# Kernel optimization log

Measured on AMD Instinct MI355X. Metric: run time of the kernel, lower is better.

## Reference

```python
import jax, jax.numpy as jnp
import numpy as np

N = 50000      # nodes
DIM = 128      # feature dim
H = 4          # heads
C = DIM // H   # per-head channels
E = 800000     # edges (before self-loops)
LRELU_SLOPE = 0.2
LN_EPS = 1e-5


def setup_inputs() -> dict:
    key = jax.random.key(0)
    ks = jax.random.split(key, 12)
    def p(k, shape, scale=0.05):
        return jax.random.normal(k, shape, jnp.float32) * scale
    return {
        "x": jax.random.normal(ks[0], (N, DIM), jnp.float32),
        "edge_index": jax.random.randint(ks[1], (2, E), 0, N),
        "W1": p(ks[2], (DIM, DIM)), "b1": jnp.zeros((DIM,), jnp.float32),
        "att_src1": p(ks[3], (H, C)), "att_dst1": p(ks[4], (H, C)),
        "W2": p(ks[5], (DIM, DIM)), "b2": jnp.zeros((DIM,), jnp.float32),
        "att_src2": p(ks[6], (H, C)), "att_dst2": p(ks[7], (H, C)),
        "gate_W": p(ks[8], (2 * DIM, 2)), "gate_b": jnp.zeros((2,), jnp.float32),
        "ln_gamma": jnp.ones((DIM,), jnp.float32), "ln_beta": jnp.zeros((DIM,), jnp.float32),
    }


def _gat(x, src, dst, W, b, a_src, a_dst):
    # Linear transform, split heads: [N, H, C]
    h = (x @ W).reshape(-1, H, C)
    # Per-node attention logits per head: [N, H]
    e_src = jnp.einsum("nhc,hc->nh", h, a_src)
    e_dst = jnp.einsum("nhc,hc->nh", h, a_dst)
    # Per-edge logits (edge j->i: src=j, dst=i): [E, H]
    e = jax.nn.leaky_relu(e_src[src] + e_dst[dst], LRELU_SLOPE)
    # Segment softmax over edges sharing a destination (self-loops guarantee >=1 edge/node)
    m = jax.ops.segment_max(e, dst, num_segments=N)
    p = jnp.exp(e - m[dst])
    s = jax.ops.segment_sum(p, dst, num_segments=N)
    alpha = p / s[dst]                                   # [E, H]
    # Weighted scatter-add aggregation
    out = jax.ops.segment_sum(h[src] * alpha[..., None], dst, num_segments=N)
    return out.reshape(-1, H * C) + b                    # [N, DIM]


def reference(x, edge_index, W1, b1, att_src1, att_dst1, W2, b2, att_src2, att_dst2,
              gate_W, gate_b, ln_gamma, ln_beta):
    n = x.shape[0]
    loops = jnp.arange(n, dtype=edge_index.dtype)
    src = jnp.concatenate([edge_index[0], loops])  # PyG GATConv add_self_loops=True
    dst = jnp.concatenate([edge_index[1], loops])
    out1 = _gat(x, src, dst, W1, b1, att_src1, att_dst1)
    out2 = _gat(x, src, dst, W2, b2, att_src2, att_dst2)
    gate = jax.nn.softmax(jnp.concatenate([out1, out2], axis=-1) @ gate_W + gate_b, axis=-1)
    out = gate[:, 0:1] * out1 + gate[:, 1:2] * out2
    # residual + LayerNorm (dropout is identity in eval)
    y = x + out
    mu = jnp.mean(y, axis=-1, keepdims=True)
    var = jnp.var(y, axis=-1, keepdims=True)
    return (y - mu) * jax.lax.rsqrt(var + LN_EPS) * ln_gamma + ln_beta
```

## Files before the change

### kernel.cpp

```cpp
#include <hip/hip_runtime.h>
#include <hip/hip_bf16.h>


typedef unsigned short u16;
typedef __bf16 bf16x8 __attribute__((ext_vector_type(8)));
typedef float f32x4 __attribute__((ext_vector_type(4)));

#define LRELU_SLOPE 0.2f
#define LN_EPS 1e-5f
#define SH 8

__device__ __forceinline__ float bfbits(unsigned int hi_bits) {
    union { unsigned int i; float f; } v; v.i = hi_bits; return v.f;
}
__device__ __forceinline__ float bflo(unsigned int u) { return bfbits(u << 16); }
__device__ __forceinline__ float bfhi(unsigned int u) { return bfbits(u & 0xFFFF0000u); }
__device__ __forceinline__ u16 f2bf(float f) {
    union { float f; unsigned int i; } v; v.f = f;
    unsigned int lsb = (v.i >> 16) & 1u;
    v.i += 0x7FFFu + lsb;
    return (u16)(v.i >> 16);
}

__global__ void k_prep(const float* __restrict__ W1, const float* __restrict__ W2,
                       u16* __restrict__ wb, int* __restrict__ deg8, int n) {
    int i = blockIdx.x * 256 + threadIdx.x;
    if (i < 32768) {
        int col = i >> 7, k = i & 127;
        float v = (col < 128) ? W1[k * 128 + col] : W2[k * 128 + (col - 128)];
        wb[i] = f2bf(v);
    }
    if (i < n) {
#pragma unroll
        for (int x = 0; x < SH; x++) deg8[x * n + i] = 0;
    }
}

__global__ __launch_bounds__(256) void k_cg(const float* __restrict__ x,
                                            const u16* __restrict__ wb,
                                            unsigned int* __restrict__ hbp, int n,
                                            const int* __restrict__ ei,
                                            int* __restrict__ deg8, int E, int Gg) {
    if ((int)blockIdx.x >= Gg) {
        int i = ((int)blockIdx.x - Gg) * 256 + threadIdx.x;
        if (i < E) {
            int sh = (i >> 8) & (SH - 1);
            atomicAdd(&deg8[sh * n + ei[E + i]], 1);
        }
        return;
    }
    int wave = threadIdx.x >> 6, lane = threadIdx.x & 63;
    int quad = lane >> 4, r16 = lane & 15;
    int row = blockIdx.x * 64 + wave * 16 + r16;
    int arow = (row < n) ? row : n - 1;
    const float* xp = x + (size_t)arow * 128 + quad * 8;
    union { u16 u[8]; bf16x8 b; } ar;
    bf16x8 a[4];
#pragma unroll
    for (int ks = 0; ks < 4; ks++) {
        float4 lo = *(const float4*)(xp + ks * 32);
        float4 hi = *(const float4*)(xp + ks * 32 + 4);
        ar.u[0] = f2bf(lo.x); ar.u[1] = f2bf(lo.y); ar.u[2] = f2bf(lo.z); ar.u[3] = f2bf(lo.w);
        ar.u[4] = f2bf(hi.x); ar.u[5] = f2bf(hi.y); ar.u[6] = f2bf(hi.z); ar.u[7] = f2bf(hi.w);
        a[ks] = ar.b;
    }
    f32x4 acc[16];
#pragma unroll
    for (int t = 0; t < 16; t++) acc[t] = (f32x4){0.f, 0.f, 0.f, 0.f};
    const u16* bbase = wb + r16 * 128 + quad * 8;
#pragma unroll
    for (int t = 0; t < 16; t++) {
        const u16* bp = bbase + t * 2048;
#pragma unroll
        for (int ks = 0; ks < 4; ks++) {
            bf16x8 b = *(const bf16x8*)(bp + ks * 32);
            acc[t] = __builtin_amdgcn_mfma_f32_16x16x32_bf16(a[ks], b, acc[t], 0, 0, 0);
        }
    }
    int row0 = blockIdx.x * 64 + wave * 16 + quad * 4;
#pragma unroll
    for (int t = 0; t < 8; t++) {
        int c = t * 16 + r16;
#pragma unroll
        for (int g = 0; g < 4; g++) {
            int gr = row0 + g;
            if (gr < n) {
                unsigned int pv = ((unsigned int)f2bf(acc[t + 8][g]) << 16) | f2bf(acc[t][g]);
                hbp[(size_t)gr * 128 + c] = pv;
            }
        }
    }
}

__global__ void k_lb(const unsigned int* __restrict__ hbp,
                     const float* __restrict__ as1, const float* __restrict__ ad1,
                     const float* __restrict__ as2, const float* __restrict__ ad2,
                     float* __restrict__ es, float* __restrict__ ed, int n,
                     const int* __restrict__ deg8, int* __restrict__ bsum, int Gl) {
    __shared__ int s[256];
    if ((int)blockIdx.x >= Gl) {
        int bid = (int)blockIdx.x - Gl;
        int i = bid * 256 + threadIdx.x;
        int v = 0;
        if (i < n) {
#pragma unroll
            for (int x = 0; x < SH; x++) v += deg8[x * n + i];
        }
        s[threadIdx.x] = v;
        __syncthreads();
        for (int o = 128; o; o >>= 1) {
            if (threadIdx.x < o) s[threadIdx.x] += s[threadIdx.x + o];
            __syncthreads();
        }
        if (threadIdx.x == 0) bsum[bid] = s[0];
        return;
    }
    int i = blockIdx.x * 256 + threadIdx.x;
    if (i >= n * 4) return;
    int node = i >> 2, head = i & 3;
    const uint4* hv = (const uint4*)(hbp + (size_t)node * 128 + head * 32);
    const float* a1 = as1 + head * 32;
    const float* d1 = ad1 + head * 32;
    const float* a2 = as2 + head * 32;
    const float* d2 = ad2 + head * 32;
    float s1 = 0.f, t1 = 0.f, s2 = 0.f, t2 = 0.f;
#pragma unroll
    for (int q = 0; q < 8; q++) {
        uint4 w = hv[q];
        unsigned int ws[4] = {w.x, w.y, w.z, w.w};
#pragma unroll
        for (int h = 0; h < 4; h++) {
            int c = q * 4 + h;
            float v1 = bflo(ws[h]), v2 = bfhi(ws[h]);
            s1 += v1 * a1[c]; t1 += v1 * d1[c];
            s2 += v2 * a2[c]; t2 += v2 * d2[c];
        }
    }
    es[node * 8 + head]     = s1;
    ed[node * 8 + head]     = t1;
    es[node * 8 + 4 + head] = s2;
    ed[node * 8 + 4 + head] = t2;
}

__global__ void k_scan(int* __restrict__ deg8, const int* __restrict__ bsum,
                       int* __restrict__ offs, int nb, int n) {
    __shared__ int s[256];
    __shared__ int bp;
    int t = threadIdx.x;
    int bv = (t < nb) ? bsum[t] : 0;
    s[t] = bv;
    __syncthreads();
    for (int o = 1; o < 256; o <<= 1) {
        int u = (t >= o) ? s[t - o] : 0;
        __syncthreads();
        s[t] += u;
        __syncthreads();
    }
    if (t == (int)blockIdx.x) bp = s[t] - bv;
    __syncthreads();
    int i = blockIdx.x * 256 + t;
    int d[SH];
    int v = 0;
    if (i < n) {
#pragma unroll
        for (int x = 0; x < SH; x++) { d[x] = deg8[x * n + i]; v += d[x]; }
    }
    s[t] = v;
    __syncthreads();
    for (int o = 1; o < 256; o <<= 1) {
        int u = (t >= o) ? s[t - o] : 0;
        __syncthreads();
        s[t] += u;
        __syncthreads();
    }
    if (i < n) {
        int e = bp + s[t] - v;
        offs[i] = e;
        int run = e;
#pragma unroll
        for (int x = 0; x < SH; x++) { deg8[x * n + i] = run; run += d[x]; }
        if (i == n - 1) offs[n] = e + v;
    }
}

__global__ void k_fill(const int* __restrict__ ei, int* __restrict__ cursor8,
                       const float* __restrict__ es, const float* __restrict__ ed,
                       int* __restrict__ ssrc, uint4* __restrict__ w, int E, int n) {
    int i = blockIdx.x * 256 + threadIdx.x;
    if (i >= E) return;
    int s = ei[i], d = ei[E + i];
    int sh = (i >> 8) & (SH - 1);
    int pos = atomicAdd(&cursor8[sh * n + d], 1);
    ssrc[pos] = s;
    float4 eslo = *(const float4*)(es + s * 8);
    float4 eshi = *(const float4*)(es + s * 8 + 4);
    float4 edlo = *(const float4*)(ed + d * 8);
    float4 edhi = *(const float4*)(ed + d * 8 + 4);
    float e1[4] = {eslo.x + edlo.x, eslo.y + edlo.y, eslo.z + edlo.z, eslo.w + edlo.w};
    float e2[4] = {eshi.x + edhi.x, eshi.y + edhi.y, eshi.z + edhi.z, eshi.w + edhi.w};
    unsigned int uw[4];
#pragma unroll
    for (int h = 0; h < 4; h++) {
        float a = e1[h]; a = (a > 0.f) ? a : LRELU_SLOPE * a;
        float b = e2[h]; b = (b > 0.f) ? b : LRELU_SLOPE * b;
        uw[h] = ((unsigned int)f2bf(__expf(b)) << 16) | f2bf(__expf(a));
    }
    w[pos] = make_uint4(uw[0], uw[1], uw[2], uw[3]);
}

__device__ __forceinline__ float wred(float v) {
#pragma unroll
    for (int off = 32; off; off >>= 1) v += __shfl_xor(v, off, 64);
    return v;
}

__device__ __forceinline__ unsigned int hsel(uint4 w, int head) {
    unsigned int r = (head == 0) ? w.x : (head == 1) ? w.y : (head == 2) ? w.z : w.w;
    return r;
}

__global__ __launch_bounds__(256) void k_agg(
    const int* __restrict__ offs, const int* __restrict__ ssrc,
    const unsigned int* __restrict__ hbp, const uint4* __restrict__ w4,
    const float* __restrict__ es, const float* __restrict__ ed,
    const float* __restrict__ b1, const float* __restrict__ b2,
    const float* __restrict__ gW, const float* __restrict__ gb,
    const float* __restrict__ x, const float* __restrict__ gamma,
    const float* __restrict__ beta, float* __restrict__ out, int n) {
    int wave = threadIdx.x >> 6, lane = threadIdx.x & 63;
    int node = blockIdx.x * 4 + wave;
    if (node >= n) return;
    node = __builtin_amdgcn_readfirstlane(node);

    int ca = lane * 2, cb = ca + 1;
    int head = lane >> 4;

    const float* esp = es + node * 8;
    const float* edp = ed + node * 8;
    float e1s = esp[head] + edp[head];
    float e2s = esp[4 + head] + edp[4 + head];
    e1s = (e1s > 0.f) ? e1s : LRELU_SLOPE * e1s;
    e2s = (e2s > 0.f) ? e2s : LRELU_SLOPE * e2s;
    float w1s = __expf(e1s), w2s = __expf(e2s);
    uint2 qs = *(const uint2*)(hbp + (size_t)node * 128 + ca);
    float l1 = w1s, l2 = w2s;
    float a1a = w1s * bflo(qs.x), a1b = w1s * bflo(qs.y);
    float a2a = w2s * bfhi(qs.x), a2b = w2s * bfhi(qs.y);

    int beg = offs[node], end = offs[node + 1];
    int k = beg;
#define ACC(wp, q) { \
        float ww1 = bflo(wp), ww2 = bfhi(wp); \
        l1 += ww1; l2 += ww2; \
        a1a += ww1 * bflo(q.x); a1b += ww1 * bflo(q.y); \
        a2a += ww2 * bfhi(q.x); a2b += ww2 * bfhi(q.y); }
    for (; k + 3 < end; k += 4) {
        int j0 = ssrc[k], j1 = ssrc[k + 1], j2 = ssrc[k + 2], j3 = ssrc[k + 3];
        uint4 w0 = w4[k], w1v = w4[k + 1], w2v = w4[k + 2], w3v = w4[k + 3];
        uint2 q0 = *(const uint2*)(hbp + (size_t)j0 * 128 + ca);
        uint2 q1 = *(const uint2*)(hbp + (size_t)j1 * 128 + ca);
        uint2 q2 = *(const uint2*)(hbp + (size_t)j2 * 128 + ca);
        uint2 q3 = *(const uint2*)(hbp + (size_t)j3 * 128 + ca);
        unsigned int wp0 = hsel(w0, head), wp1 = hsel(w1v, head);
        unsigned int wp2 = hsel(w2v, head), wp3 = hsel(w3v, head);
        ACC(wp0, q0) ACC(wp1, q1) ACC(wp2, q2) ACC(wp3, q3)
    }
    for (; k < end; k++) {
        int j = ssrc[k];
        uint4 wv = w4[k];
        uint2 q = *(const uint2*)(hbp + (size_t)j * 128 + ca);
        unsigned int wp = hsel(wv, head);
        ACC(wp, q)
    }
#undef ACC

    float2 b1v = *(const float2*)(b1 + ca);
    float2 b2v = *(const float2*)(b2 + ca);
    float r1 = 1.f / l1, r2 = 1.f / l2;
    float o1a = a1a * r1 + b1v.x;
    float o1b = a1b * r1 + b1v.y;
    float o2a = a2a * r2 + b2v.x;
    float o2b = a2b * r2 + b2v.y;

    float2 g1a = *(const float2*)(gW + 2 * ca);
    float2 g1b = *(const float2*)(gW + 2 * cb);
    float2 g2a = *(const float2*)(gW + 2 * (128 + ca));
    float2 g2b = *(const float2*)(gW + 2 * (128 + cb));
    float p0 = o1a * g1a.x + o1b * g1b.x + o2a * g2a.x + o2b * g2b.x;
    float p1 = o1a * g1a.y + o1b * g1b.y + o2a * g2a.y + o2b * g2b.y;
    p0 = wred(p0) + gb[0];
    p1 = wred(p1) + gb[1];
    float mg = fmaxf(p0, p1);
    float eg0 = __expf(p0 - mg), eg1 = __expf(p1 - mg);
    float g0 = eg0 / (eg0 + eg1), g1 = 1.f - g0;

    float2 xv = *(const float2*)(x + (size_t)node * 128 + ca);
    float ya = xv.x + g0 * o1a + g1 * o2a;
    float yb = xv.y + g0 * o1b + g1 * o2b;

    float s  = wred(ya + yb);
    float ss = wred(ya * ya + yb * yb);
    float mean = s * (1.f / 128.f);
    float var  = ss * (1.f / 128.f) - mean * mean;
    float rstd = rsqrtf(var + LN_EPS);
    float2 gv = *(const float2*)(gamma + ca);
    float2 bv = *(const float2*)(beta + ca);
    float2 ov;
    ov.x = (ya - mean) * rstd * gv.x + bv.x;
    ov.y = (yb - mean) * rstd * gv.y + bv.y;
    *(float2*)(out + (size_t)node * 128 + ca) = ov;
}

extern "C" void kernel_launch(void* const* d_in, const int* in_sizes, int n_in,
                              void* d_out, int out_size, void* d_ws, size_t ws_size,
                              hipStream_t stream) {
    const float* x   = (const float*)d_in[0];
    const int*   ei  = (const int*)d_in[1];
    const float* W1  = (const float*)d_in[2];
    const float* b1  = (const float*)d_in[3];
    const float* as1 = (const float*)d_in[4];
    const float* ad1 = (const float*)d_in[5];
    const float* W2  = (const float*)d_in[6];
    const float* b2  = (const float*)d_in[7];
    const float* as2 = (const float*)d_in[8];
    const float* ad2 = (const float*)d_in[9];
    const float* gW  = (const float*)d_in[10];
    const float* gb  = (const float*)d_in[11];
    const float* gamma = (const float*)d_in[12];
    const float* beta  = (const float*)d_in[13];
    float* out = (float*)d_out;

    int n = in_sizes[0] / 128;
    int E = in_sizes[1] / 2;

    char* p = (char*)d_ws;
    auto take = [&](size_t bytes) {
        char* q = p;
        p += (bytes + 255) & ~(size_t)255;
        return (void*)q;
    };
    u16* wb    = (u16*)take((size_t)256 * 128 * 2);
    unsigned int* hbp = (unsigned int*)take((size_t)n * 128 * 4);
    float* es  = (float*)take((size_t)n * 8 * 4);
    float* ed  = (float*)take((size_t)n * 8 * 4);
    int* deg8  = (int*)take((size_t)SH * n * 4);
    int* offs  = (int*)take((size_t)(n + 1) * 4);
    int* bsum  = (int*)take((size_t)256 * 4);
    int* ssrc  = (int*)take((size_t)E * 4);
    uint4* w   = (uint4*)take((size_t)E * 16);

    int nb = (n + 255) / 256;
    int Gg = (n + 63) / 64;
    int Gc = (E + 255) / 256;
    int Gl = (n * 4 + 255) / 256;

    k_prep<<<nb, 256, 0, stream>>>(W1, W2, wb, deg8, n);
    k_cg<<<Gg + Gc, 256, 0, stream>>>(x, wb, hbp, n, ei, deg8, E, Gg);
    k_lb<<<Gl + nb, 256, 0, stream>>>(hbp, as1, ad1, as2, ad2, es, ed, n,
                                      deg8, bsum, Gl);
    k_scan<<<nb, 256, 0, stream>>>(deg8, bsum, offs, nb, n);
    k_fill<<<Gc, 256, 0, stream>>>(ei, deg8, es, ed, ssrc, w, E, n);
    k_agg<<<(n + 3) / 4, 256, 0, stream>>>(offs, ssrc, hbp, w, es, ed,
                                           b1, b2, gW, gb, x, gamma, beta, out, n);
}
```

Measured before the change: 273.1 us.

## Fuse preprocessing kernels into one cooperative persistent kernel with grid syncs

Replaces the five preprocessing launches (weight convert, GEMM plus degree count, logits plus block sums, scan, CSR fill) with a single cooperative kernel that runs each phase in grid-stride loops separated by grid.sync(). The aim is to remove per-launch overhead and the gaps between kernels. The grid is capped at 512 blocks with __launch_bounds__(256,2), which may cut parallelism for the GEMM and atomic phases. The grid-wide barriers also add their own cost. The old multi-kernel path is kept as a fallback if the cooperative launch fails.

```diff
diff --git a/kernel.cpp b/kernel.cpp
--- a/kernel.cpp
+++ b/kernel.cpp
@@ -1,5 +1,8 @@
 #include <hip/hip_runtime.h>
 #include <hip/hip_bf16.h>
+#include <hip/hip_cooperative_groups.h>
+
+namespace cg = cooperative_groups;
 
 
 typedef unsigned short u16;
@@ -22,14 +25,233 @@
     return (u16)(v.i >> 16);
 }
 
+
+__device__ __forceinline__ void ph_wb(int i, const float* __restrict__ W1,
+                                      const float* __restrict__ W2,
+                                      u16* __restrict__ wb) {
+    int col = i >> 7, k = i & 127;
+    float v = (col < 128) ? W1[k * 128 + col] : W2[k * 128 + (col - 128)];
+    wb[i] = f2bf(v);
+}
+
+__device__ __forceinline__ void ph_gemm(int t0, int tid, const float* __restrict__ x,
+                                        const u16* __restrict__ wb,
+                                        unsigned int* __restrict__ hbp, int n) {
+    int wave = tid >> 6, lane = tid & 63;
+    int quad = lane >> 4, r16 = lane & 15;
+    int row = t0 * 64 + wave * 16 + r16;
+    int arow = (row < n) ? row : n - 1;
+    const float* xp = x + (size_t)arow * 128 + quad * 8;
+    union { u16 u[8]; bf16x8 b; } ar;
+    bf16x8 af[4];
+#pragma unroll
+    for (int ks = 0; ks < 4; ks++) {
+        float4 lo = *(const float4*)(xp + ks * 32);
+        float4 hi = *(const float4*)(xp + ks * 32 + 4);
+        ar.u[0] = f2bf(lo.x); ar.u[1] = f2bf(lo.y); ar.u[2] = f2bf(lo.z); ar.u[3] = f2bf(lo.w);
+        ar.u[4] = f2bf(hi.x); ar.u[5] = f2bf(hi.y); ar.u[6] = f2bf(hi.z); ar.u[7] = f2bf(hi.w);
+        af[ks] = ar.b;
+    }
+    f32x4 acc[16];
+#pragma unroll
+    for (int t = 0; t < 16; t++) acc[t] = (f32x4){0.f, 0.f, 0.f, 0.f};
+    const u16* bbase = wb + r16 * 128 + quad * 8;
+#pragma unroll
+    for (int t = 0; t < 16; t++) {
+        const u16* bptr = bbase + t * 2048;
+#pragma unroll
+        for (int ks = 0; ks < 4; ks++) {
+            bf16x8 b = *(const bf16x8*)(bptr + ks * 32);
+            acc[t] = __builtin_amdgcn_mfma_f32_16x16x32_bf16(af[ks], b, acc[t], 0, 0, 0);
+        }
+    }
+    int row0 = t0 * 64 + wave * 16 + quad * 4;
+#pragma unroll
+    for (int t = 0; t < 8; t++) {
+        int c = t * 16 + r16;
+#pragma unroll
+        for (int g = 0; g < 4; g++) {
+            int gr = row0 + g;
+            if (gr < n) {
+                unsigned int pv = ((unsigned int)f2bf(acc[t + 8][g]) << 16) | f2bf(acc[t][g]);
+                hbp[(size_t)gr * 128 + c] = pv;
+            }
+        }
+    }
+}
+
+__device__ __forceinline__ void ph_logits(int i, const unsigned int* __restrict__ hbp,
+                                          const float* __restrict__ as1,
+                                          const float* __restrict__ ad1,
+                                          const float* __restrict__ as2,
+                                          const float* __restrict__ ad2,
+                                          float* __restrict__ es, float* __restrict__ ed) {
+    int node = i >> 2, head = i & 3;
+    const uint4* hv = (const uint4*)(hbp + (size_t)node * 128 + head * 32);
+    const float* a1 = as1 + head * 32;
+    const float* d1 = ad1 + head * 32;
+    const float* a2 = as2 + head * 32;
+    const float* d2 = ad2 + head * 32;
+    float s1 = 0.f, t1 = 0.f, s2 = 0.f, t2 = 0.f;
+#pragma unroll
+    for (int q = 0; q < 8; q++) {
+        uint4 wv = hv[q];
+        unsigned int ws[4] = {wv.x, wv.y, wv.z, wv.w};
+#pragma unroll
+        for (int h = 0; h < 4; h++) {
+            int c = q * 4 + h;
+            float v1 = bflo(ws[h]), v2 = bfhi(ws[h]);
+            s1 += v1 * a1[c]; t1 += v1 * d1[c];
+            s2 += v2 * a2[c]; t2 += v2 * d2[c];
+        }
+    }
+    es[node * 8 + head]     = s1;
+    ed[node * 8 + head]     = t1;
+    es[node * 8 + 4 + head] = s2;
+    ed[node * 8 + 4 + head] = t2;
+}
+
+__device__ __forceinline__ void ph_bsum(int b, int tid, const int* __restrict__ deg8,
+                                        int* __restrict__ bsum, int n, int* s) {
+    int i = b * 256 + tid;
+    int v = 0;
+    if (i < n) {
+#pragma unroll
+        for (int x = 0; x < SH; x++) v += deg8[x * n + i];
+    }
+    s[tid] = v;
+    __syncthreads();
+    for (int o = 128; o; o >>= 1) {
+        if (tid < o) s[tid] += s[tid + o];
+        __syncthreads();
+    }
+    if (tid == 0) bsum[b] = s[0];
+    __syncthreads();
+}
+
+__device__ __forceinline__ void ph_scan(int b, int tid, int* __restrict__ deg8,
+                                        const int* __restrict__ bsum,
+                                        int* __restrict__ offs, int nb, int n,
+                                        int* s, int* bp) {
+    int bv = (tid < nb) ? bsum[tid] : 0;
+    s[tid] = bv;
+    __syncthreads();
+    for (int o = 1; o < 256; o <<= 1) {
+        int u = (tid >= o) ? s[tid - o] : 0;
+        __syncthreads();
+        s[tid] += u;
+        __syncthreads();
+    }
+    if (tid == b) *bp = s[tid] - bv;
+    __syncthreads();
+    int i = b * 256 + tid;
+    int d[SH];
+    int v = 0;
+    if (i < n) {
+#pragma unroll
+        for (int x = 0; x < SH; x++) { d[x] = deg8[x * n + i]; v += d[x]; }
+    }
+    s[tid] = v;
+    __syncthreads();
+    for (int o = 1; o < 256; o <<= 1) {
+        int u = (tid >= o) ? s[tid - o] : 0;
+        __syncthreads();
+        s[tid] += u;
+        __syncthreads();
+    }
+    if (i < n) {
+        int e = *bp + s[tid] - v;
+        offs[i] = e;
+        int run = e;
+#pragma unroll
+        for (int x = 0; x < SH; x++) { deg8[x * n + i] = run; run += d[x]; }
+        if (i == n - 1) offs[n] = e + v;
+    }
+    __syncthreads();
+}
+
+__device__ __forceinline__ void ph_fill(int i, const int* __restrict__ ei,
+                                        int* __restrict__ cursor8,
+                                        const float* __restrict__ es,
+                                        const float* __restrict__ ed,
+                                        int* __restrict__ ssrc, uint4* __restrict__ w,
+                                        int E, int n) {
+    int sv = ei[i], d = ei[E + i];
+    int sh = (i >> 8) & (SH - 1);
+    int pos = atomicAdd(&cursor8[sh * n + d], 1);
+    ssrc[pos] = sv;
+    float4 eslo = *(const float4*)(es + sv * 8);
+    float4 eshi = *(const float4*)(es + sv * 8 + 4);
+    float4 edlo = *(const float4*)(ed + d * 8);
+    float4 edhi = *(const float4*)(ed + d * 8 + 4);
+    float e1[4] = {eslo.x + edlo.x, eslo.y + edlo.y, eslo.z + edlo.z, eslo.w + edlo.w};
+    float e2[4] = {eshi.x + edhi.x, eshi.y + edhi.y, eshi.z + edhi.z, eshi.w + edhi.w};
+    unsigned int uw[4];
+#pragma unroll
+    for (int h = 0; h < 4; h++) {
+        float av = e1[h]; av = (av > 0.f) ? av : LRELU_SLOPE * av;
+        float bv = e2[h]; bv = (bv > 0.f) ? bv : LRELU_SLOPE * bv;
+        uw[h] = ((unsigned int)f2bf(__expf(bv)) << 16) | f2bf(__expf(av));
+    }
+    w[pos] = make_uint4(uw[0], uw[1], uw[2], uw[3]);
+}
+
+
+struct MegaArgs {
+    const float* x;
+    const int* ei;
+    const float* W1; const float* W2;
+    const float* as1; const float* ad1;
+    const float* as2; const float* ad2;
+    u16* wb;
+    unsigned int* hbp;
+    float* es; float* ed;
+    int* deg8;
+    int* offs;
+    int* bsum;
+    int* ssrc;
+    uint4* w;
+    int n, E, Gg, nb;
+};
+
+__global__ __launch_bounds__(256, 2) void k_mega(MegaArgs a) {
+    cg::grid_group grid = cg::this_grid();
+    __shared__ int s[256];
+    __shared__ int bp;
+    const int G = gridDim.x;
+    const int bid = blockIdx.x, tid = threadIdx.x;
+    const int gtid = bid * 256 + tid, gstride = G * 256;
+    const int n = a.n, E = a.E;
+
+    for (int i = gtid; i < 32768; i += gstride) ph_wb(i, a.W1, a.W2, a.wb);
+    for (int i = gtid; i < SH * n; i += gstride) a.deg8[i] = 0;
+    grid.sync();
+
+    for (int t0 = bid; t0 < a.Gg; t0 += G) ph_gemm(t0, tid, a.x, a.wb, a.hbp, n);
+    for (int i = gtid; i < E; i += gstride) {
+        int sh = (i >> 8) & (SH - 1);
+        atomicAdd(&a.deg8[sh * n + a.ei[E + i]], 1);
+    }
+    grid.sync();
+
+    for (int i = gtid; i < n * 4; i += gstride)
+        ph_logits(i, a.hbp, a.as1, a.ad1, a.as2, a.ad2, a.es, a.ed);
+    for (int b = bid; b < a.nb; b += G) ph_bsum(b, tid, a.deg8, a.bsum, n, s);
+    grid.sync();
+
+    for (int b = bid; b < a.nb; b += G)
+        ph_scan(b, tid, a.deg8, a.bsum, a.offs, a.nb, n, s, &bp);
+    grid.sync();
+
+    for (int i = gtid; i < E; i += gstride)
+        ph_fill(i, a.ei, a.deg8, a.es, a.ed, a.ssrc, a.w, E, n);
+}
+
+
 __global__ void k_prep(const float* __restrict__ W1, const float* __restrict__ W2,
                        u16* __restrict__ wb, int* __restrict__ deg8, int n) {
     int i = blockIdx.x * 256 + threadIdx.x;
-    if (i < 32768) {
-        int col = i >> 7, k = i & 127;
-        float v = (col < 128) ? W1[k * 128 + col] : W2[k * 128 + (col - 128)];
-        wb[i] = f2bf(v);
-    }
+    if (i < 32768) ph_wb(i, W1, W2, wb);
     if (i < n) {
 #pragma unroll
         for (int x = 0; x < SH; x++) deg8[x * n + i] = 0;
@@ -49,47 +271,7 @@
         }
         return;
     }
-    int wave = threadIdx.x >> 6, lane = threadIdx.x & 63;
-    int quad = lane >> 4, r16 = lane & 15;
-    int row = blockIdx.x * 64 + wave * 16 + r16;
-    int arow = (row < n) ? row : n - 1;
-    const float* xp = x + (size_t)arow * 128 + quad * 8;
-    union { u16 u[8]; bf16x8 b; } ar;
-    bf16x8 a[4];
-#pragma unroll
-    for (int ks = 0; ks < 4; ks++) {
-        float4 lo = *(const float4*)(xp + ks * 32);
-        float4 hi = *(const float4*)(xp + ks * 32 + 4);
-        ar.u[0] = f2bf(lo.x); ar.u[1] = f2bf(lo.y); ar.u[2] = f2bf(lo.z); ar.u[3] = f2bf(lo.w);
-        ar.u[4] = f2bf(hi.x); ar.u[5] = f2bf(hi.y); ar.u[6] = f2bf(hi.z); ar.u[7] = f2bf(hi.w);
-        a[ks] = ar.b;
-    }
-    f32x4 acc[16];
-#pragma unroll
-    for (int t = 0; t < 16; t++) acc[t] = (f32x4){0.f, 0.f, 0.f, 0.f};
-    const u16* bbase = wb + r16 * 128 + quad * 8;
-#pragma unroll
-    for (int t = 0; t < 16; t++) {
-        const u16* bp = bbase + t * 2048;
-#pragma unroll
-        for (int ks = 0; ks < 4; ks++) {
-            bf16x8 b = *(const bf16x8*)(bp + ks * 32);
-            acc[t] = __builtin_amdgcn_mfma_f32_16x16x32_bf16(a[ks], b, acc[t], 0, 0, 0);
-        }
-    }
-    int row0 = blockIdx.x * 64 + wave * 16 + quad * 4;
-#pragma unroll
-    for (int t = 0; t < 8; t++) {
-        int c = t * 16 + r16;
-#pragma unroll
-        for (int g = 0; g < 4; g++) {
-            int gr = row0 + g;
-            if (gr < n) {
-                unsigned int pv = ((unsigned int)f2bf(acc[t + 8][g]) << 16) | f2bf(acc[t][g]);
-                hbp[(size_t)gr * 128 + c] = pv;
-            }
-        }
-    }
+    ph_gemm(blockIdx.x, threadIdx.x, x, wb, hbp, n);
 }
 
 __global__ void k_lb(const unsigned int* __restrict__ hbp,
@@ -99,114 +281,27 @@
                      const int* __restrict__ deg8, int* __restrict__ bsum, int Gl) {
     __shared__ int s[256];
     if ((int)blockIdx.x >= Gl) {
-        int bid = (int)blockIdx.x - Gl;
-        int i = bid * 256 + threadIdx.x;
-        int v = 0;
-        if (i < n) {
-#pragma unroll
-            for (int x = 0; x < SH; x++) v += deg8[x * n + i];
-        }
-        s[threadIdx.x] = v;
-        __syncthreads();
-        for (int o = 128; o; o >>= 1) {
-            if (threadIdx.x < o) s[threadIdx.x] += s[threadIdx.x + o];
-            __syncthreads();
-        }
-        if (threadIdx.x == 0) bsum[bid] = s[0];
+        ph_bsum((int)blockIdx.x - Gl, threadIdx.x, deg8, bsum, n, s);
         return;
     }
     int i = blockIdx.x * 256 + threadIdx.x;
-    if (i >= n * 4) return;
-    int node = i >> 2, head = i & 3;
-    const uint4* hv = (const uint4*)(hbp + (size_t)node * 128 + head * 32);
-    const float* a1 = as1 + head * 32;
-    const float* d1 = ad1 + head * 32;
-    const float* a2 = as2 + head * 32;
-    const float* d2 = ad2 + head * 32;
-    float s1 = 0.f, t1 = 0.f, s2 = 0.f, t2 = 0.f;
-#pragma unroll
-    for (int q = 0; q < 8; q++) {
-        uint4 w = hv[q];
-        unsigned int ws[4] = {w.x, w.y, w.z, w.w};
-#pragma unroll
-        for (int h = 0; h < 4; h++) {
-            int c = q * 4 + h;
-            float v1 = bflo(ws[h]), v2 = bfhi(ws[h]);
-            s1 += v1 * a1[c]; t1 += v1 * d1[c];
-            s2 += v2 * a2[c]; t2 += v2 * d2[c];
-        }
-    }
-    es[node * 8 + head]     = s1;
-    ed[node * 8 + head]     = t1;
-    es[node * 8 + 4 + head] = s2;
-    ed[node * 8 + 4 + head] = t2;
+    if (i < n * 4) ph_logits(i, hbp, as1, ad1, as2, ad2, es, ed);
 }
 
 __global__ void k_scan(int* __restrict__ deg8, const int* __restrict__ bsum,
                        int* __restrict__ offs, int nb, int n) {
     __shared__ int s[256];
     __shared__ int bp;
-    int t = threadIdx.x;
-    int bv = (t < nb) ? bsum[t] : 0;
-    s[t] = bv;
-    __syncthreads();
-    for (int o = 1; o < 256; o <<= 1) {
-        int u = (t >= o) ? s[t - o] : 0;
-        __syncthreads();
-        s[t] += u;
-        __syncthreads();
-    }
-    if (t == (int)blockIdx.x) bp = s[t] - bv;
-    __syncthreads();
-    int i = blockIdx.x * 256 + t;
-    int d[SH];
-    int v = 0;
-    if (i < n) {
-#pragma unroll
-        for (int x = 0; x < SH; x++) { d[x] = deg8[x * n + i]; v += d[x]; }
-    }
-    s[t] = v;
-    __syncthreads();
-    for (int o = 1; o < 256; o <<= 1) {
-        int u = (t >= o) ? s[t - o] : 0;
-        __syncthreads();
-        s[t] += u;
-        __syncthreads();
-    }
-    if (i < n) {
-        int e = bp + s[t] - v;
-        offs[i] = e;
-        int run = e;
-#pragma unroll
-        for (int x = 0; x < SH; x++) { deg8[x * n + i] = run; run += d[x]; }
-        if (i == n - 1) offs[n] = e + v;
-    }
+    ph_scan(blockIdx.x, threadIdx.x, deg8, bsum, offs, nb, n, s, &bp);
 }
 
 __global__ void k_fill(const int* __restrict__ ei, int* __restrict__ cursor8,
                        const float* __restrict__ es, const float* __restrict__ ed,
                        int* __restrict__ ssrc, uint4* __restrict__ w, int E, int n) {
     int i = blockIdx.x * 256 + threadIdx.x;
-    if (i >= E) return;
-    int s = ei[i], d = ei[E + i];
-    int sh = (i >> 8) & (SH - 1);
-    int pos = atomicAdd(&cursor8[sh * n + d], 1);
-    ssrc[pos] = s;
-    float4 eslo = *(const float4*)(es + s * 8);
-    float4 eshi = *(const float4*)(es + s * 8 + 4);
-    float4 edlo = *(const float4*)(ed + d * 8);
-    float4 edhi = *(const float4*)(ed + d * 8 + 4);
-    float e1[4] = {eslo.x + edlo.x, eslo.y + edlo.y, eslo.z + edlo.z, eslo.w + edlo.w};
-    float e2[4] = {eshi.x + edhi.x, eshi.y + edhi.y, eshi.z + edhi.z, eshi.w + edhi.w};
-    unsigned int uw[4];
-#pragma unroll
-    for (int h = 0; h < 4; h++) {
-        float a = e1[h]; a = (a > 0.f) ? a : LRELU_SLOPE * a;
-        float b = e2[h]; b = (b > 0.f) ? b : LRELU_SLOPE * b;
-        uw[h] = ((unsigned int)f2bf(__expf(b)) << 16) | f2bf(__expf(a));
-    }
-    w[pos] = make_uint4(uw[0], uw[1], uw[2], uw[3]);
-}
+    if (i < E) ph_fill(i, ei, cursor8, es, ed, ssrc, w, E, n);
+}
+
 
 __device__ __forceinline__ float wred(float v) {
 #pragma unroll
@@ -298,9 +393,9 @@
     float ya = xv.x + g0 * o1a + g1 * o2a;
     float yb = xv.y + g0 * o1b + g1 * o2b;
 
-    float s  = wred(ya + yb);
+    float sm = wred(ya + yb);
     float ss = wred(ya * ya + yb * yb);
-    float mean = s * (1.f / 128.f);
+    float mean = sm * (1.f / 128.f);
     float var  = ss * (1.f / 128.f) - mean * mean;
     float rstd = rsqrtf(var + LN_EPS);
     float2 gv = *(const float2*)(gamma + ca);
@@ -354,12 +449,32 @@
     int Gc = (E + 255) / 256;
     int Gl = (n * 4 + 255) / 256;
 
-    k_prep<<<nb, 256, 0, stream>>>(W1, W2, wb, deg8, n);
-    k_cg<<<Gg + Gc, 256, 0, stream>>>(x, wb, hbp, n, ei, deg8, E, Gg);
-    k_lb<<<Gl + nb, 256, 0, stream>>>(hbp, as1, ad1, as2, ad2, es, ed, n,
-                                      deg8, bsum, Gl);
-    k_scan<<<nb, 256, 0, stream>>>(deg8, bsum, offs, nb, n);
-    k_fill<<<Gc, 256, 0, stream>>>(ei, deg8, es, ed, ssrc, w, E, n);
+    MegaArgs a;
+    a.x = x; a.ei = ei; a.W1 = W1; a.W2 = W2;
+    a.as1 = as1; a.ad1 = ad1; a.as2 = as2; a.ad2 = ad2;
+    a.wb = wb; a.hbp = hbp; a.es = es; a.ed = ed;
+    a.deg8 = deg8; a.offs = offs; a.bsum = bsum; a.ssrc = ssrc; a.w = w;
+    a.n = n; a.E = E; a.Gg = Gg; a.nb = nb;
+
+    int maxB = 0;
+    hipError_t qerr = hipOccupancyMaxActiveBlocksPerMultiprocessor(
+        &maxB, (const void*)k_mega, 256, 0);
+    hipError_t lerr = hipErrorUnknown;
+    if (qerr == hipSuccess && maxB > 0) {
+        int G = maxB * 256;
+        if (G > 512) G = 512;
+        void* params[] = { &a };
+        lerr = hipLaunchCooperativeKernel((const void*)k_mega, dim3(G), dim3(256),
+                                          params, 0, stream);
+    }
+    if (lerr != hipSuccess) {
+        k_prep<<<nb, 256, 0, stream>>>(W1, W2, wb, deg8, n);
+        k_cg<<<Gg + Gc, 256, 0, stream>>>(x, wb, hbp, n, ei, deg8, E, Gg);
+        k_lb<<<Gl + nb, 256, 0, stream>>>(hbp, as1, ad1, as2, ad2, es, ed, n,
+                                          deg8, bsum, Gl);
+        k_scan<<<nb, 256, 0, stream>>>(deg8, bsum, offs, nb, n);
+        k_fill<<<Gc, 256, 0, stream>>>(ei, deg8, es, ed, ssrc, w, E, n);
+    }
     k_agg<<<(n + 3) / 4, 256, 0, stream>>>(offs, ssrc, hbp, w, es, ed,
                                            b1, b2, gW, gb, x, gamma, beta, out, n);
 }
```

New measurement: 434.5 us. 59.1% more time.
